# Performance work log

Hardware: AMD Instinct MI355X
Metric: run time of the kernel (lower is better)

Reference implementation:

```python
import jax, jax.numpy as jnp
import numpy as np

EPSILON = 1.0
SIGMA = 1.0
SPRING_CONSTANT = 0.5


def setup_inputs() -> dict:
    key = jax.random.key(0)
    x = jax.random.normal(key, (4, 2048, 3), dtype=jnp.float32)
    return {"x": x}


def _pairwise_offdiag_distances(x):
    # x: (B, N, D) -> distances between all ordered pairs, diagonal removed: (B, N, N-1)
    B, N, D = x.shape
    pair_vec = x[:, :, None, :] - x[:, None, :, :]          # (B, N, N, D)
    sq = jnp.sum(pair_vec * pair_vec, axis=-1)              # (B, N, N)
    # safe sqrt (diagonal is exactly zero; it is sliced away below)
    dist = jnp.where(sq == 0, 0.0, jnp.sqrt(jnp.where(sq == 0, 1.0, sq)))
    # reshape trick from the torch source: drop the diagonal entries
    d = dist.reshape(B, N * N)[:, 1:]
    d = d.reshape(B, N - 1, N + 1)[:, :, :-1]
    return d.reshape(B, N, N - 1)                           # (B, N, N-1)


def reference(x):
    # Lennard-Jones potential (cutoff=None branch) + harmonic confinement;
    # forward() returns log_prob = -potential.
    d = _pairwise_offdiag_distances(x)                      # (B, N, N-1), all > 0
    inv = 1.0 / d
    pow6 = (SIGMA * inv) ** 6
    pair_potential = EPSILON * 4.0 * (pow6 * pow6 - pow6)
    # source multiplies by distances_inverse * distances (identity here, kept fused away)
    total_potential = jnp.sum(pair_potential, axis=(-1, -2)) / 2.0   # (B,)
    # harmonic potential about the center of mass (periodic=False)
    com = jnp.mean(x, axis=-2, keepdims=True)
    rel = x - com
    harm = 0.5 * SPRING_CONSTANT * jnp.sum(rel * rel, axis=(-1, -2))  # (B,)
    return -(total_potential + harm)
```

## Files before the change

### kernel.cpp

```cpp
#include <hip/hip_runtime.h>


#define NPART 2048
#define BATCH 4
#define TI 256
#define TJ 64
#define CI (NPART / TI)
#define CJ (NPART / TJ)
#define SPRING_K 0.5f

template <bool GUARD>
__device__ __forceinline__ float pair_chunk(const float* __restrict__ xj,
                                            float xi, float yi, float zi,
                                            int i_rel) {
    float acc = 0.0f;
#pragma unroll
    for (int jj = 0; jj < TJ; ++jj) {
        const float dx = xi - xj[3 * jj + 0];
        const float dy = yi - xj[3 * jj + 1];
        const float dz = zi - xj[3 * jj + 2];
        const float sq = fmaf(dx, dx, fmaf(dy, dy, dz * dz));
        const float inv2 = __builtin_amdgcn_rcpf(sq);
        const float p6 = inv2 * inv2 * inv2;
        const float term = fmaf(p6, p6, -p6);
        if (GUARD) {
            acc += (jj == i_rel) ? 0.0f : term;
        } else {
            acc += term;
        }
    }
    return acc;
}

__global__ __launch_bounds__(256) void lj_pairs(const float* __restrict__ x,
                                                float* __restrict__ partial) {
    const int t  = threadIdx.x;
    const int ib = blockIdx.x;
    const int jb = blockIdx.y;
    const int b  = blockIdx.z;
    const float* __restrict__ xb = x + (size_t)b * NPART * 3;

    const int i = ib * TI + t;
    const float xi = xb[3 * i + 0];
    const float yi = xb[3 * i + 1];
    const float zi = xb[3 * i + 2];

    const int jbase = jb * TJ;
    const float* __restrict__ xj = xb + 3 * jbase;
    const bool overlap = (jbase >= ib * TI) && (jbase < ib * TI + TI);

    float acc = overlap ? pair_chunk<true >(xj, xi, yi, zi, i - jbase)
                        : pair_chunk<false>(xj, xi, yi, zi, 0);
    acc *= 4.0f;

    for (int o = 32; o > 0; o >>= 1) acc += __shfl_down(acc, o, 64);
    __shared__ float wsum[4];
    const int lane = t & 63, w = t >> 6;
    if (lane == 0) wsum[w] = acc;
    __syncthreads();
    if (t == 0) {
        partial[((size_t)b * CI + ib) * CJ + jb] = wsum[0] + wsum[1] + wsum[2] + wsum[3];
    }
}

__global__ __launch_bounds__(256) void lj_finish(const float* __restrict__ x,
                                                 const float* __restrict__ partial,
                                                 float* __restrict__ out) {
    const int b = blockIdx.x;
    const int t = threadIdx.x;
    const float* __restrict__ xb = x + (size_t)b * NPART * 3;

    float sp = 0.0f;
    if (t < CI * CJ) sp = partial[(size_t)b * CI * CJ + t];

    float sxv = 0.0f, syv = 0.0f, szv = 0.0f, s2 = 0.0f;
    for (int i = t; i < NPART; i += 256) {
        const float xv = xb[3 * i + 0];
        const float yv = xb[3 * i + 1];
        const float zv = xb[3 * i + 2];
        sxv += xv; syv += yv; szv += zv;
        s2 = fmaf(xv, xv, fmaf(yv, yv, fmaf(zv, zv, s2)));
    }

    for (int o = 32; o > 0; o >>= 1) {
        sp  += __shfl_down(sp,  o, 64);
        sxv += __shfl_down(sxv, o, 64);
        syv += __shfl_down(syv, o, 64);
        szv += __shfl_down(szv, o, 64);
        s2  += __shfl_down(s2,  o, 64);
    }

    __shared__ float red[4][5];
    const int lane = t & 63, w = t >> 6;
    if (lane == 0) {
        red[w][0] = sp; red[w][1] = sxv; red[w][2] = syv; red[w][3] = szv; red[w][4] = s2;
    }
    __syncthreads();
    if (t == 0) {
        float SP = 0, SX = 0, SY = 0, SZ = 0, S2 = 0;
        for (int k = 0; k < 4; ++k) {
            SP += red[k][0]; SX += red[k][1]; SY += red[k][2]; SZ += red[k][3]; S2 += red[k][4];
        }
        const float pair = 0.5f * SP;
        const float harm = 0.5f * SPRING_K * (S2 - (SX * SX + SY * SY + SZ * SZ) * (1.0f / NPART));
        out[b] = -(pair + harm);
    }
}

extern "C" void kernel_launch(void* const* d_in, const int* in_sizes, int n_in,
                              void* d_out, int out_size, void* d_ws, size_t ws_size,
                              hipStream_t stream) {
    const float* x = (const float*)d_in[0];
    float* out = (float*)d_out;
    float* partial = (float*)d_ws;

    dim3 grid(CI, CJ, BATCH);
    lj_pairs<<<grid, 256, 0, stream>>>(x, partial);
    lj_finish<<<BATCH, 256, 0, stream>>>(x, partial, out);
}
```

Baseline: 62.48 us.

## Exploit pair symmetry with upper-triangular tiles and fuse the finish via atomics

Only the upper-triangular tile pairs (j > i) are computed, using a closed-form mapping from block index to (ib, jb) tile. The diagonal tiles keep only pairs with j above i, which halves the pairwise LJ work, so the 0.5 double-count factor is dropped. The second reduction kernel is removed: block 0 of each batch also computes the harmonic term, and every block atomically adds its negated partial sum into the output. This saves a kernel launch and the partial-buffer round trip. In exchange, the result depends on the output being zeroed before launch, and float atomics make the summation order nondeterministic.

```diff
diff --git a/kernel.cpp b/kernel.cpp
--- a/kernel.cpp
+++ b/kernel.cpp
@@ -5,8 +5,7 @@
 #define BATCH 4
 #define TI 256
 #define TJ 64
-#define CI (NPART / TI)
-#define CJ (NPART / TJ)
+#define NTILES 144
 #define SPRING_K 0.5f
 
 template <bool GUARD>
@@ -24,7 +23,7 @@
         const float p6 = inv2 * inv2 * inv2;
         const float term = fmaf(p6, p6, -p6);
         if (GUARD) {
-            acc += (jj == i_rel) ? 0.0f : term;
+            acc += (jj > i_rel) ? term : 0.0f;
         } else {
             acc += term;
         }
@@ -32,13 +31,27 @@
     return acc;
 }
 
-__global__ __launch_bounds__(256) void lj_pairs(const float* __restrict__ x,
-                                                float* __restrict__ partial) {
-    const int t  = threadIdx.x;
-    const int ib = blockIdx.x;
-    const int jb = blockIdx.y;
-    const int b  = blockIdx.z;
+__global__ __launch_bounds__(256) void lj_fused(const float* __restrict__ x,
+                                                float* __restrict__ out) {
+    const int t = threadIdx.x;
+    const int f = blockIdx.x;
+    const int b = blockIdx.y;
     const float* __restrict__ xb = x + (size_t)b * NPART * 3;
+
+    int ib, jb;
+    bool guard;
+    if (f < 32) {
+        ib = f >> 2;
+        jb = (ib << 2) + (f & 3);
+        guard = true;
+    } else {
+        int g = f - 32;
+        int ibb = 0, pre = 0;
+        while (g >= pre + 28 - 4 * ibb) { pre += 28 - 4 * ibb; ++ibb; }
+        ib = ibb;
+        jb = ((ib + 1) << 2) + (g - pre);
+        guard = false;
+    }
 
     const int i = ib * TI + t;
     const float xi = xb[3 * i + 0];
@@ -47,11 +60,45 @@
 
     const int jbase = jb * TJ;
     const float* __restrict__ xj = xb + 3 * jbase;
-    const bool overlap = (jbase >= ib * TI) && (jbase < ib * TI + TI);
 
-    float acc = overlap ? pair_chunk<true >(xj, xi, yi, zi, i - jbase)
-                        : pair_chunk<false>(xj, xi, yi, zi, 0);
-    acc *= 4.0f;
+    float acc = guard ? pair_chunk<true >(xj, xi, yi, zi, i - jbase)
+                      : pair_chunk<false>(xj, xi, yi, zi, 0);
+    acc *= -4.0f;
+
+    if (f == 0) {
+        float sxv = 0.0f, syv = 0.0f, szv = 0.0f, s2 = 0.0f;
+#pragma unroll
+        for (int k = 0; k < NPART / TI; ++k) {
+            const int p = k * TI + t;
+            const float xv = xb[3 * p + 0];
+            const float yv = xb[3 * p + 1];
+            const float zv = xb[3 * p + 2];
+            sxv += xv; syv += yv; szv += zv;
+            s2 = fmaf(xv, xv, fmaf(yv, yv, fmaf(zv, zv, s2)));
+        }
+        for (int o = 32; o > 0; o >>= 1) {
+            sxv += __shfl_down(sxv, o, 64);
+            syv += __shfl_down(syv, o, 64);
+            szv += __shfl_down(szv, o, 64);
+            s2  += __shfl_down(s2,  o, 64);
+        }
+        __shared__ float hred[4][4];
+        const int lane = t & 63, w = t >> 6;
+        if (lane == 0) {
+            hred[w][0] = sxv; hred[w][1] = syv; hred[w][2] = szv; hred[w][3] = s2;
+        }
+        __syncthreads();
+        if (t == 0) {
+            float SX = 0, SY = 0, SZ = 0, S2 = 0;
+            for (int k = 0; k < 4; ++k) {
+                SX += hred[k][0]; SY += hred[k][1]; SZ += hred[k][2]; S2 += hred[k][3];
+            }
+            const float harm = 0.5f * SPRING_K *
+                (S2 - (SX * SX + SY * SY + SZ * SZ) * (1.0f / NPART));
+            acc -= harm;
+        }
+        __syncthreads();
+    }
 
     for (int o = 32; o > 0; o >>= 1) acc += __shfl_down(acc, o, 64);
     __shared__ float wsum[4];
@@ -59,51 +106,7 @@
     if (lane == 0) wsum[w] = acc;
     __syncthreads();
     if (t == 0) {
-        partial[((size_t)b * CI + ib) * CJ + jb] = wsum[0] + wsum[1] + wsum[2] + wsum[3];
-    }
-}
-
-__global__ __launch_bounds__(256) void lj_finish(const float* __restrict__ x,
-                                                 const float* __restrict__ partial,
-                                                 float* __restrict__ out) {
-    const int b = blockIdx.x;
-    const int t = threadIdx.x;
-    const float* __restrict__ xb = x + (size_t)b * NPART * 3;
-
-    float sp = 0.0f;
-    if (t < CI * CJ) sp = partial[(size_t)b * CI * CJ + t];
-
-    float sxv = 0.0f, syv = 0.0f, szv = 0.0f, s2 = 0.0f;
-    for (int i = t; i < NPART; i += 256) {
-        const float xv = xb[3 * i + 0];
-        const float yv = xb[3 * i + 1];
-        const float zv = xb[3 * i + 2];
-        sxv += xv; syv += yv; szv += zv;
-        s2 = fmaf(xv, xv, fmaf(yv, yv, fmaf(zv, zv, s2)));
-    }
-
-    for (int o = 32; o > 0; o >>= 1) {
-        sp  += __shfl_down(sp,  o, 64);
-        sxv += __shfl_down(sxv, o, 64);
-        syv += __shfl_down(syv, o, 64);
-        szv += __shfl_down(szv, o, 64);
-        s2  += __shfl_down(s2,  o, 64);
-    }
-
-    __shared__ float red[4][5];
-    const int lane = t & 63, w = t >> 6;
-    if (lane == 0) {
-        red[w][0] = sp; red[w][1] = sxv; red[w][2] = syv; red[w][3] = szv; red[w][4] = s2;
-    }
-    __syncthreads();
-    if (t == 0) {
-        float SP = 0, SX = 0, SY = 0, SZ = 0, S2 = 0;
-        for (int k = 0; k < 4; ++k) {
-            SP += red[k][0]; SX += red[k][1]; SY += red[k][2]; SZ += red[k][3]; S2 += red[k][4];
-        }
-        const float pair = 0.5f * SP;
-        const float harm = 0.5f * SPRING_K * (S2 - (SX * SX + SY * SY + SZ * SZ) * (1.0f / NPART));
-        out[b] = -(pair + harm);
+        atomicAdd(&out[b], wsum[0] + wsum[1] + wsum[2] + wsum[3]);
     }
 }
 
@@ -112,9 +115,7 @@
                               hipStream_t stream) {
     const float* x = (const float*)d_in[0];
     float* out = (float*)d_out;
-    float* partial = (float*)d_ws;
 
-    dim3 grid(CI, CJ, BATCH);
-    lj_pairs<<<grid, 256, 0, stream>>>(x, partial);
-    lj_finish<<<BATCH, 256, 0, stream>>>(x, partial, out);
+    dim3 grid(NTILES, BATCH);
+    lj_fused<<<grid, 256, 0, stream>>>(x, out);
 }
```

Result: no change. 61.30 us (-1.9%).
